# Optimization experiments

Measured on AMD Instinct MI355X. Metric: run time of the kernel, lower is better.

Reference implementation:

```python
import jax, jax.numpy as jnp
import numpy as np

B, D, R = 256, 4096, 16
MAX_R = 2 * R - 1  # static upper bound on radius; per-row steps masked by r_mask


def setup_inputs() -> dict:
    key = jax.random.key(0)
    kx, kw, kb = jax.random.split(key, 3)
    x = (jax.random.uniform(kx, (B, D)) < 0.5).astype(jnp.float32)  # random bits
    A = jax.random.normal(kw, (D, D), dtype=jnp.float32) * 0.01
    W = (A + A.T) * 0.5  # symmetric quadratic coupling
    bias = jax.random.normal(kb, (D,), dtype=jnp.float32) * 0.1
    return {"x": x, "W": W, "bias": bias}


def reference(x, W, bias):
    # energy model: score(x) = 0.5 * x' W x + b' x  (per batch row)
    score_fn = lambda z: 0.5 * jnp.einsum('bd,de,be->b', z, W, z) + z @ bias
    grad_fn = jax.grad(lambda z: score_fn(z).sum())

    key = jax.random.key(42)
    k_rad, k_samp, k_acc = jax.random.split(key, 3)
    radius = jax.random.randint(k_rad, (B, 1), 1, 2 * R)
    r_mask = (jnp.arange(MAX_R)[None, :] < radius).astype(x.dtype)  # [B, MAX_R]

    score_x = score_fn(x)                                  # [B]
    grad_x = jax.lax.stop_gradient(grad_fn(x))             # detach as in torch
    score_change_x = (1.0 - 2.0 * x) * grad_x * 0.5        # [B, D] proposal logits

    b_idx = jnp.arange(B)

    def body(carry, inp):
        cur_x, blocked = carry
        k, m = inp  # per-step RNG key, per-step mask column [B]
        idx = jax.random.categorical(k, score_change_x + blocked)  # multinomial w/ zeroed probs
        cur_bits = cur_x[b_idx, idx]
        cur_x = cur_x.at[b_idx, idx].set(m * (1.0 - cur_bits) + (1.0 - m) * cur_bits)
        blocked = blocked.at[b_idx, idx].set(-jnp.inf)  # prob_x[b, idx] = 0
        return (cur_x, blocked), idx

    keys = jax.random.split(k_samp, MAX_R)
    (y, _), idx_steps = jax.lax.scan(body, (x, jnp.zeros_like(x)), (keys, r_mask.T))
    idx_all = idx_steps.T  # [B, MAX_R]

    score_y = score_fn(y)
    grad_y = jax.lax.stop_gradient(grad_fn(y))
    score_change_y = (1.0 - 2.0 * y) * grad_y * 0.5

    # masked log-softmax tensors: step j's proposal excludes indices flipped at other steps
    oh = jax.nn.one_hot(idx_all, D, dtype=x.dtype)        # [B, MAX_R, D]
    cum = jnp.cumsum(oh, axis=1)
    before = cum - oh                                      # indices sampled at steps i < j
    after = cum[:, -1:, :] - cum                           # indices sampled at steps i > j
    change_fwd = jnp.where(before > 0, -jnp.inf, score_change_x[:, None, :])
    change_bwd = jnp.where(after > 0, -jnp.inf, score_change_y[:, None, :])

    g_fwd = jnp.take_along_axis(jax.nn.log_softmax(change_fwd, axis=-1), idx_all[:, :, None], axis=2)[..., 0]
    g_bwd = jnp.take_along_axis(jax.nn.log_softmax(change_bwd, axis=-1), idx_all[:, :, None], axis=2)[..., 0]
    log_fwd = jnp.sum(g_fwd * r_mask, axis=-1) + score_x
    log_bwd = jnp.sum(g_bwd * r_mask, axis=-1) + score_y

    log_acc = log_bwd - log_fwd
    u = jax.random.uniform(k_acc, (B,))
    accepted = (jnp.exp(log_acc) >= u).astype(x.dtype)[:, None]  # [B, 1]
    y_sg = jax.lax.stop_gradient(y)
    acc_sg = jax.lax.stop_gradient(accepted)
    return y_sg * acc_sg + (1.0 - acc_sg) * x
```

## Files before the change

### kernel.cpp

```cpp
#include <hip/hip_runtime.h>
#include <math.h>

#define BB 256
#define DD 4096
#define MAXR 31
#define NCAND 4
#define CAPG 192
#define U_THRESH 0.9778f
#define GUARD 4.0f

typedef unsigned short u16;
typedef u16 u16x8 __attribute__((ext_vector_type(8)));
typedef __bf16 bf16x8 __attribute__((ext_vector_type(8)));
typedef float f32x16 __attribute__((ext_vector_type(16)));

__device__ __forceinline__ void tf2x32(unsigned k0, unsigned k1, unsigned c0, unsigned c1,
                                       unsigned &o0, unsigned &o1) {
  unsigned ks2 = k0 ^ k1 ^ 0x1BD11BDAu;
  unsigned x0 = c0 + k0;
  unsigned x1 = c1 + k1;
#define TF_ROT(v, r) (((v) << (r)) | ((v) >> (32 - (r))))
#define TF_R(r) { x0 += x1; x1 = TF_ROT(x1, r); x1 ^= x0; }
  TF_R(13) TF_R(15) TF_R(26) TF_R(6)   x0 += k1;  x1 += ks2 + 1u;
  TF_R(17) TF_R(29) TF_R(16) TF_R(24)  x0 += ks2; x1 += k0 + 2u;
  TF_R(13) TF_R(15) TF_R(26) TF_R(6)   x0 += k0;  x1 += k1 + 3u;
  TF_R(17) TF_R(29) TF_R(16) TF_R(24)  x0 += k1;  x1 += ks2 + 4u;
  TF_R(13) TF_R(15) TF_R(26) TF_R(6)   x0 += ks2; x1 += k0 + 5u;
#undef TF_R
#undef TF_ROT
  o0 = x0; o1 = x1;
}

__device__ __forceinline__ unsigned tf_xor(unsigned k0, unsigned k1, unsigned c0, unsigned c1) {
  unsigned a, b; tf2x32(k0, k1, c0, c1, a, b); return a ^ b;
}

__device__ __forceinline__ float bits_to_unit(unsigned bits) {
  return __uint_as_float(0x3f800000u | (bits >> 9)) - 1.0f;
}

__device__ __forceinline__ void keys_of(int j, unsigned &kk0, unsigned &kk1) {
  unsigned ks0, ks1;
  tf2x32(0u, 42u, 0u, 1u, ks0, ks1);
  tf2x32(ks0, ks1, 0u, (unsigned)j, kk0, kk1);
}

__device__ __forceinline__ int radius_of(int b) {
  unsigned krad0, krad1, k10, k11, k20, k21;
  tf2x32(0u, 42u, 0u, 0u, krad0, krad1);
  tf2x32(krad0, krad1, 0u, 0u, k10, k11);
  tf2x32(krad0, krad1, 0u, 1u, k20, k21);
  unsigned hi = tf_xor(k10, k11, 0u, (unsigned)b);
  unsigned lo = tf_xor(k20, k21, 0u, (unsigned)b);
  return 1 + (int)(((hi % 31u) * 4u + (lo % 31u)) % 31u);
}

__device__ __forceinline__ float uacc_of(int b) {
  unsigned ka0, ka1;
  tf2x32(0u, 42u, 0u, 2u, ka0, ka1);
  return bits_to_unit(tf_xor(ka0, ka1, 0u, (unsigned)b));
}

__device__ __forceinline__ double dlog(double x) {
  unsigned long long ub = (unsigned long long)__double_as_longlong(x);
  int e = (int)((ub >> 52) & 0x7FFull) - 1022;
  double m = __longlong_as_double((long long)((ub & 0x000FFFFFFFFFFFFFull) | 0x3FE0000000000000ull));
  if (m < 0.70710678118654752440) { m *= 2.0; e -= 1; }
  double r = (m - 1.0) / (m + 1.0);
  double z = r * r;
  double s = fma(z, fma(z, fma(z, fma(z, fma(z, fma(z, 1.0/15.0, 1.0/13.0),
                1.0/11.0), 1.0/9.0), 1.0/7.0), 1.0/5.0), 1.0/3.0);
  double t2 = 2.0 * r;
  return fma((double)e, 0.69314718055994530942, fma(t2 * z, s, t2));
}

__device__ __forceinline__ float gumbel_from_u(float f) {
  float uu = (f == 0.0f) ? 1.17549435e-38f : f;
  float t1 = (float)dlog((double)uu);
  return -(float)dlog((double)(-t1));
}

__device__ __forceinline__ float gumbel_of(unsigned kk0, unsigned kk1, unsigned n) {
  return gumbel_from_u(bits_to_unit(tf_xor(kk0, kk1, 0u, n)));
}

__device__ __forceinline__ double blockReduce1024(double v, double* lds) {
  int t = threadIdx.x;
  #pragma unroll
  for (int off = 32; off > 0; off >>= 1) v += __shfl_down(v, off);
  __syncthreads();
  if ((t & 63) == 0) lds[t >> 6] = v;
  __syncthreads();
  double s = 0.0;
  #pragma unroll
  for (int i = 0; i < 16; i++) s += lds[i];
  return s;
}

__device__ __forceinline__ void split3(float w, u16 &h, u16 &l, u16 &q) {
  __bf16 hb = (__bf16)w;
  float r = w - (float)hb;
  __bf16 lb = (__bf16)r;
  float r2 = r - (float)lb;
  __bf16 qb = (__bf16)r2;
  h = __builtin_bit_cast(u16, hb);
  l = __builtin_bit_cast(u16, lb);
  q = __builtin_bit_cast(u16, qb);
}

__global__ __launch_bounds__(256, 2) void k_mega(
    const float* __restrict__ x, const float* __restrict__ W,
    float* __restrict__ Cpart, int klen, int ngemm,
    u16* __restrict__ flt_list, int* __restrict__ flt_cnt) {
  int t = threadIdx.x;

  if ((int)blockIdx.x < ngemm) {
    int g = blockIdx.x;
    int nt = g & 63, mt = (g >> 6) & 1, kc = g >> 7;
    int k0 = kc * klen;

    __shared__ alignas(16) u16 As[4][128][8];
    __shared__ alignas(16) u16 Bs[3][4][64][8];

    const float* xrow = x + (size_t)(mt * 128) * DD + k0;
    const float* wrow = W + (size_t)(nt * 64) * DD + k0;

    int am = t >> 2, akg = t & 3;
    int bn = t >> 2, bkg = t & 3;

    float4 aR0, aR1, aR2, aR3;
    float4 bR0, bR1;
    int nsteps = klen / 32;

    {
      const float* ap = xrow + (size_t)am * DD + akg * 8;
      aR0 = *(const float4*)ap;       aR1 = *(const float4*)(ap + 4);
      const float* ap2 = ap + (size_t)64 * DD;
      aR2 = *(const float4*)ap2;      aR3 = *(const float4*)(ap2 + 4);
      const float* wp = wrow + (size_t)bn * DD + bkg * 8;
      bR0 = *(const float4*)wp;       bR1 = *(const float4*)(wp + 4);
    }

    int wid = t >> 6, lane = t & 63;
    int wr = (wid >> 1) * 64, wc = (wid & 1) * 32;
    int lm = lane & 31, lh = lane >> 5;

    f32x16 acc[2];
    #pragma unroll
    for (int i = 0; i < 2; i++)
      #pragma unroll
      for (int r = 0; r < 16; r++) acc[i][r] = 0.0f;

    for (int s = 0; s < nsteps; s++) {
      __syncthreads();
      {
        float af32[8];
        *(float4*)&af32[0] = aR0; *(float4*)&af32[4] = aR1;
        u16x8 av;
        #pragma unroll
        for (int i = 0; i < 8; i++) av[i] = __builtin_bit_cast(u16, (__bf16)af32[i]);
        *(u16x8*)&As[akg][am][0] = av;
        *(float4*)&af32[0] = aR2; *(float4*)&af32[4] = aR3;
        #pragma unroll
        for (int i = 0; i < 8; i++) av[i] = __builtin_bit_cast(u16, (__bf16)af32[i]);
        *(u16x8*)&As[akg][am + 64][0] = av;
      }
      {
        float wv[8];
        *(float4*)&wv[0] = bR0; *(float4*)&wv[4] = bR1;
        u16x8 ph, pl, pq;
        #pragma unroll
        for (int i = 0; i < 8; i++) {
          u16 hh, ll, qq;
          split3(wv[i], hh, ll, qq);
          ph[i] = hh; pl[i] = ll; pq[i] = qq;
        }
        *(u16x8*)&Bs[0][bkg][bn][0] = ph;
        *(u16x8*)&Bs[1][bkg][bn][0] = pl;
        *(u16x8*)&Bs[2][bkg][bn][0] = pq;
      }
      __syncthreads();
      if (s + 1 < nsteps) {
        int kk = (s + 1) * 32;
        const float* ap = xrow + (size_t)am * DD + kk + akg * 8;
        aR0 = *(const float4*)ap;       aR1 = *(const float4*)(ap + 4);
        const float* ap2 = ap + (size_t)64 * DD;
        aR2 = *(const float4*)ap2;      aR3 = *(const float4*)(ap2 + 4);
        const float* wp = wrow + (size_t)bn * DD + kk + bkg * 8;
        bR0 = *(const float4*)wp;       bR1 = *(const float4*)(wp + 4);
      }
      bf16x8 af[2][2];
      #pragma unroll
      for (int mf = 0; mf < 2; mf++)
        #pragma unroll
        for (int h = 0; h < 2; h++)
          af[mf][h] = *(const bf16x8*)&As[2 * h + lh][wr + mf * 32 + lm][0];
      __builtin_amdgcn_s_setprio(1);
      #pragma unroll
      for (int p = 0; p < 3; p++) {
        bf16x8 b0 = *(const bf16x8*)&Bs[p][lh][wc + lm][0];
        bf16x8 b1 = *(const bf16x8*)&Bs[p][2 + lh][wc + lm][0];
        #pragma unroll
        for (int mf = 0; mf < 2; mf++) {
          acc[mf] = __builtin_amdgcn_mfma_f32_32x32x16_bf16(af[mf][0], b0, acc[mf], 0, 0, 0);
          acc[mf] = __builtin_amdgcn_mfma_f32_32x32x16_bf16(af[mf][1], b1, acc[mf], 0, 0, 0);
        }
      }
      __builtin_amdgcn_s_setprio(0);
    }

    float* Cp = Cpart + (size_t)kc * ((size_t)BB * DD);
    #pragma unroll
    for (int mf = 0; mf < 2; mf++) {
      int col   = nt * 64 + wc + lm;
      int rbase = mt * 128 + wr + mf * 32 + 4 * lh;
      #pragma unroll
      for (int r = 0; r < 16; r++) {
        int row = rbase + (r & 3) + 8 * (r >> 2);
        Cp[(size_t)row * DD + col] = acc[mf][r];
      }
    }
  } else {
    int fb = (int)blockIdx.x - ngemm;
    int b = fb / MAXR, j = fb % MAXR;
    unsigned kk0, kk1;
    keys_of(j, kk0, kk1);
    unsigned base_c = (unsigned)(b * DD);
    const unsigned KMIN = (unsigned)ceil((double)U_THRESH * 8388608.0);

    __shared__ int fcnt;
    __shared__ u16 fl[CAPG];
    if (t == 0) fcnt = 0;
    __syncthreads();

    #pragma unroll
    for (int p = 0; p < 16; p++) {
      int d = t + 256 * p;
      unsigned bits = tf_xor(kk0, kk1, 0u, base_c + (unsigned)d);
      if ((bits >> 9) >= KMIN) {
        int pos = atomicAdd(&fcnt, 1);
        if (pos < CAPG) fl[pos] = (u16)d;
      }
    }
    __syncthreads();
    int n = fcnt;
    if (t == 0) flt_cnt[fb] = n;
    int nstore = n < CAPG ? n : CAPG;
    if (t < nstore) flt_list[(size_t)fb * CAPG + t] = fl[t];
  }
}

__global__ __launch_bounds__(1024) void k_tail(
    const float* __restrict__ Cpart, const float* __restrict__ bias,
    const float* __restrict__ x, const float* __restrict__ W,
    const u16* __restrict__ flt_list, const int* __restrict__ flt_cnt,
    float* __restrict__ out, int KS) {
  int b = blockIdx.x, t = threadIdx.x;

  __shared__ float sc_lds[DD];
  __shared__ float gr_lds[DD];
  __shared__ double redbuf[16];
  __shared__ float lmx[16];
  __shared__ float ls_v[16];
  __shared__ int   ls_i[16];
  __shared__ float win_v[4];
  __shared__ int   win_i[4];
  __shared__ int   cand_lds[MAXR][NCAND];
  __shared__ int   fb_list[MAXR];
  __shared__ int   nfb_s;
  __shared__ int   fidx[MAXR];
  __shared__ float fsgn[MAXR];
  __shared__ unsigned mask[DD / 32];
  __shared__ int   pick_s;
  __shared__ int   nf_s;
  __shared__ float scmax_s;
  __shared__ double score_x_s, score_y_s, Ssum_s, Tsum_s;
  __shared__ float scx_s[MAXR], scy_s[MAXR];
  __shared__ float accf;

  int d0 = t * 4;
  size_t o = (size_t)b * DD + d0;
  float a0 = 0.f, a1 = 0.f, a2 = 0.f, a3 = 0.f;
  for (int kc = 0; kc < KS; kc++) {
    float4 c = *(const float4*)&Cpart[(size_t)kc * BB * DD + o];
    a0 += c.x; a1 += c.y; a2 += c.z; a3 += c.w;
  }
  float4 bv4 = *(const float4*)&bias[d0];
  float4 xv4 = *(const float4*)&x[o];
  float gg[4] = { a0 + bv4.x, a1 + bv4.y, a2 + bv4.z, a3 + bv4.w };
  float xx[4] = { xv4.x, xv4.y, xv4.z, xv4.w };
  float bb[4] = { bv4.x, bv4.y, bv4.z, bv4.w };
  float scv[4];
  double s1 = 0.0, s2 = 0.0;
  float mx = -INFINITY;
  #pragma unroll
  for (int k = 0; k < 4; k++) {
    scv[k] = (1.0f - 2.0f * xx[k]) * gg[k] * 0.5f;
    mx = fmaxf(mx, scv[k]);
    s1 += (double)xx[k] * (double)gg[k];
    s2 += (double)xx[k] * (double)bb[k];
  }
  *(float4*)&sc_lds[d0] = *(float4*)&scv[0];
  *(float4*)&gr_lds[d0] = *(float4*)&gg[0];
  if (t < 128) mask[t] = 0u;
  if (t == 0) { nf_s = radius_of(b); nfb_s = 0; }
  double sx = exp((double)scv[0]) + exp((double)scv[1]) + exp((double)scv[2]) + exp((double)scv[3]);
  double S1 = blockReduce1024(s1, redbuf);
  double S2 = blockReduce1024(s2, redbuf);
  double Sv = blockReduce1024(sx, redbuf);
  #pragma unroll
  for (int off = 32; off > 0; off >>= 1) mx = fmaxf(mx, __shfl_down(mx, off));
  __syncthreads();
  if ((t & 63) == 0) lmx[t >> 6] = mx;
  __syncthreads();
  if (t == 0) {
    float m = lmx[0];
    #pragma unroll
    for (int i = 1; i < 16; i++) m = fmaxf(m, lmx[i]);
    score_x_s = 0.5 * (S1 + S2);
    scmax_s = m;
    Ssum_s = Sv;
  }
  __syncthreads();

  int g = t >> 8, tg = t & 255;
  float scmax_l = scmax_s;
  for (int jj = 0; jj < 8; jj++) {
    int j = jj * 4 + g;
    bool active = (j < MAXR);
    unsigned kk0 = 0, kk1 = 0;
    int n = 0;
    if (active) {
      keys_of(j, kk0, kk1);
      n = flt_cnt[b * MAXR + j];
    }
    bool fastok = active && !(n > CAPG || n < NCAND);
    float v = -INFINITY; int di = 0x7FFFFFFF;
    bool dead = true;
    if (fastok && tg < n) {
      int d = (int)flt_list[(size_t)(b * MAXR + j) * CAPG + tg];
      float f = bits_to_unit(tf_xor(kk0, kk1, 0u, (unsigned)(b * DD) + (unsigned)d));
      v = sc_lds[d] + gumbel_from_u(f);
      di = d;
      dead = false;
    }
    float v4 = -INFINITY;
    for (int r = 0; r < NCAND; r++) {
      float bv = dead ? -INFINITY : v;
      int   bi = dead ? 0x7FFFFFFF : di;
      #pragma unroll
      for (int off = 32; off > 0; off >>= 1) {
        float ov = __shfl_down(bv, off);
        int   oi = __shfl_down(bi, off);
        if (ov > bv || (ov == bv && oi < bi)) { bv = ov; bi = oi; }
      }
      if ((t & 63) == 0) { ls_v[t >> 6] = bv; ls_i[t >> 6] = bi; }
      __syncthreads();
      if (tg == 0 && fastok) {
        float fv = ls_v[4 * g]; int fi = ls_i[4 * g];
        #pragma unroll
        for (int w = 1; w < 4; w++)
          if (ls_v[4 * g + w] > fv || (ls_v[4 * g + w] == fv && ls_i[4 * g + w] < fi)) { fv = ls_v[4 * g + w]; fi = ls_i[4 * g + w]; }
        win_v[g] = fv; win_i[g] = fi;
        cand_lds[j][r] = fi;
      }
      __syncthreads();
      if (fastok) {
        v4 = win_v[g];
        if (di == win_i[g]) dead = true;
      }
    }
    if (active && tg == 0) {
      bool needfb = !fastok || (v4 < scmax_l + GUARD);
      if (needfb) fb_list[atomicAdd(&nfb_s, 1)] = j;
    }
    __syncthreads();
  }

  int nfb = nfb_s;
  for (int fi = 0; fi < nfb; fi++) {
    int j = fb_list[fi];
    unsigned kk0, kk1;
    keys_of(j, kk0, kk1);
    float vq[4]; int dq[4];
    unsigned alive = 0xFu;
    #pragma unroll
    for (int q = 0; q < 4; q++) {
      int d = t * 4 + q;
      vq[q] = sc_lds[d] + gumbel_of(kk0, kk1, (unsigned)(b * DD + d));
      dq[q] = d;
    }
    for (int r = 0; r < NCAND; r++) {
      float lv = -INFINITY; int li = 0x7FFFFFFF;
      #pragma unroll
      for (int q = 0; q < 4; q++)
        if (((alive >> q) & 1u) && (vq[q] > lv || (vq[q] == lv && dq[q] < li))) { lv = vq[q]; li = dq[q]; }
      #pragma unroll
      for (int off = 32; off > 0; off >>= 1) {
        float ov = __shfl_down(lv, off);
        int   oi = __shfl_down(li, off);
        if (ov > lv || (ov == lv && oi < li)) { lv = ov; li = oi; }
      }
      if ((t & 63) == 0) { ls_v[t >> 6] = lv; ls_i[t >> 6] = li; }
      __syncthreads();
      if (t == 0) {
        float fv = ls_v[0]; int fi2 = ls_i[0];
        #pragma unroll
        for (int w = 1; w < 16; w++)
          if (ls_v[w] > fv || (ls_v[w] == fv && ls_i[w] < fi2)) { fv = ls_v[w]; fi2 = ls_i[w]; }
        cand_lds[j][r] = fi2;
        win_i[0] = fi2;
      }
      __syncthreads();
      int wi = win_i[0];
      #pragma unroll
      for (int q = 0; q < 4; q++) if (dq[q] == wi) alive &= ~(1u << q);
    }
    __syncthreads();
  }

  int jdone = 0;
  while (true) {
    if (t == 0) {
      int j = jdone;
      while (j < MAXR) {
        int pick = -1;
        #pragma unroll
        for (int r = 0; r < NCAND; r++) {
          int idx = cand_lds[j][r];
          if (pick < 0 && !((mask[idx >> 5] >> (idx & 31)) & 1u)) pick = idx;
        }
        if (pick < 0) break;
        fidx[j] = pick;
        mask[pick >> 5] |= (1u << (pick & 31));
        j++;
      }
      pick_s = j;
    }
    __syncthreads();
    int jf = pick_s;
    if (jf >= MAXR) break;
    {
      unsigned kk0, kk1;
      keys_of(jf, kk0, kk1);
      float lv = -INFINITY; int li = 0x7FFFFFFF;
      #pragma unroll
      for (int q = 0; q < 4; q++) {
        int d = t * 4 + q;
        if ((mask[d >> 5] >> (d & 31)) & 1u) continue;
        float vv = sc_lds[d] + gumbel_of(kk0, kk1, (unsigned)(b * DD + d));
        if (vv > lv || (vv == lv && d < li)) { lv = vv; li = d; }
      }
      #pragma unroll
      for (int off = 32; off > 0; off >>= 1) {
        float ov = __shfl_down(lv, off);
        int   oi = __shfl_down(li, off);
        if (ov > lv || (ov == lv && oi < li)) { lv = ov; li = oi; }
      }
      if ((t & 63) == 0) { ls_v[t >> 6] = lv; ls_i[t >> 6] = li; }
      __syncthreads();
      if (t == 0) {
        float fv = ls_v[0]; int fi2 = ls_i[0];
        #pragma unroll
        for (int w = 1; w < 16; w++)
          if (ls_v[w] > fv || (ls_v[w] == fv && ls_i[w] < fi2)) { fv = ls_v[w]; fi2 = ls_i[w]; }
        fidx[jf] = fi2;
        mask[fi2 >> 5] |= (1u << (fi2 & 31));
      }
      __syncthreads();
    }
    jdone = jf + 1;
  }

  int nf = nf_s;
  if (t < nf) fsgn[t] = 1.0f - 2.0f * x[(size_t)b * DD + fidx[t]];
  __syncthreads();

  float gd[4] = { gr_lds[d0], gr_lds[d0 + 1], gr_lds[d0 + 2], gr_lds[d0 + 3] };
  float yy[4] = { xx[0], xx[1], xx[2], xx[3] };
  for (int jj = 0; jj < nf; jj++) {
    int fd = fidx[jj];
    float s = fsgn[jj];
    float4 wv = *(const float4*)&W[(size_t)fd * DD + d0];
    gd[0] = fmaf(s, wv.x, gd[0]);
    gd[1] = fmaf(s, wv.y, gd[1]);
    gd[2] = fmaf(s, wv.z, gd[2]);
    gd[3] = fmaf(s, wv.w, gd[3]);
    int r = fd - d0;
    if (r >= 0 && r < 4) yy[r] = 1.0f - xx[r];
  }
  float scy[4];
  double t1 = 0.0, t2 = 0.0;
  #pragma unroll
  for (int k = 0; k < 4; k++) {
    scy[k] = (1.0f - 2.0f * yy[k]) * gd[k] * 0.5f;
    t1 += (double)yy[k] * (double)gd[k];
    t2 += (double)yy[k] * (double)bb[k];
  }
  double sy = exp((double)scy[0]) + exp((double)scy[1]) + exp((double)scy[2]) + exp((double)scy[3]);
  __syncthreads();
  *(float4*)&gr_lds[d0] = *(float4*)&scy[0];
  double T1 = blockReduce1024(t1, redbuf);
  double T2 = blockReduce1024(t2, redbuf);
  double Tv = blockReduce1024(sy, redbuf);
  if (t == 0) { score_y_s = 0.5 * (T1 + T2); Tsum_s = Tv; }
  __syncthreads();

  if (t < MAXR) {
    int id = fidx[t];
    scx_s[t] = sc_lds[id];
    scy_s[t] = gr_lds[id];
  }
  __syncthreads();
  if (t < 32) {
    int lane = t;
    double S = Ssum_s, T = Tsum_s;
    double ex = (t < MAXR) ? exp((double)scx_s[t]) : 0.0;
    double scn = ex;
    #pragma unroll
    for (int off = 1; off < 32; off <<= 1) {
      double ov = __shfl_up(scn, off);
      if (lane >= off) scn += ov;
    }
    double pre = scn - ex;
    double gf = (t < nf) ? ((double)scx_s[t] - dlog(S - pre)) : 0.0;
    double ey = (t < MAXR) ? exp((double)scy_s[t]) : 0.0;
    double scn2 = ey;
    #pragma unroll
    for (int off = 1; off < 32; off <<= 1) {
      double ov = __shfl_down(scn2, off);
      if (lane + off < 32) scn2 += ov;
    }
    double suf = scn2 - ey;
    double gb = (t < nf) ? ((double)scy_s[t] - dlog(T - suf)) : 0.0;
    #pragma unroll
    for (int off = 16; off > 0; off >>= 1) {
      gf += __shfl_down(gf, off);
      gb += __shfl_down(gb, off);
    }
    if (t == 0) {
      double log_acc = (gb + score_y_s) - (gf + score_x_s);
      accf = (exp(log_acc) >= (double)uacc_of(b)) ? 1.0f : 0.0f;
    }
  }
  __syncthreads();
  float a = accf;
  float4 ov4;
  ov4.x = a * yy[0] + (1.0f - a) * xx[0];
  ov4.y = a * yy[1] + (1.0f - a) * xx[1];
  ov4.z = a * yy[2] + (1.0f - a) * xx[2];
  ov4.w = a * yy[3] + (1.0f - a) * xx[3];
  *(float4*)&out[o] = ov4;
}

extern "C" void kernel_launch(void* const* d_in, const int* in_sizes, int n_in,
                              void* d_out, int out_size, void* d_ws, size_t ws_size,
                              hipStream_t stream) {
  const float* x    = (const float*)d_in[0];
  const float* W    = (const float*)d_in[1];
  const float* bias = (const float*)d_in[2];
  float* out = (float*)d_out;
  char* ws = (char*)d_ws;
  const size_t MB = 1ull << 20;

  u16*    flt_list = (u16*)(ws + 0*MB);
  int*    flt_cnt  = (int*)(ws + 3*MB);
  float*  Cpart    = (float*)(ws + 4*MB);

  size_t base = 4*MB;
  int KS = 1;
  if      (ws_size >= base + 16*MB) KS = 4;
  else if (ws_size >= base +  8*MB) KS = 2;

  int NG = 64 * 2 * KS;

  k_mega<<<NG + BB*MAXR, 256, 0, stream>>>(x, W, Cpart, DD/KS, NG, flt_list, flt_cnt);
  k_tail<<<BB, 1024, 0, stream>>>(Cpart, bias, x, W, flt_list, flt_cnt, out, KS);
}
```

Measured before the change: 239.5 us.

## Split mega kernel into filter and GEMM launches; wave-per-step candidate selection

The combined GEMM+filter kernel is split into two separate launches, k_filter then k_gemm, and the setprio hints around the MFMA loop are dropped. In k_tail, top-NCAND candidate selection now gives each wave its own proposal step, using xor-shuffle reductions over three values per lane. This replaces the four-wave groups that needed block-wide syncs on every round. It removes many __syncthreads from the tail but adds a kernel launch and loses the overlap of filter blocks with GEMM blocks.

```diff
diff --git a/kernel.cpp b/kernel.cpp
--- a/kernel.cpp
+++ b/kernel.cpp
@@ -108,146 +108,144 @@
   q = __builtin_bit_cast(u16, qb);
 }
 
-__global__ __launch_bounds__(256, 2) void k_mega(
+__global__ __launch_bounds__(256, 2) void k_gemm(
     const float* __restrict__ x, const float* __restrict__ W,
-    float* __restrict__ Cpart, int klen, int ngemm,
-    u16* __restrict__ flt_list, int* __restrict__ flt_cnt) {
+    float* __restrict__ Cpart, int klen) {
   int t = threadIdx.x;
-
-  if ((int)blockIdx.x < ngemm) {
-    int g = blockIdx.x;
-    int nt = g & 63, mt = (g >> 6) & 1, kc = g >> 7;
-    int k0 = kc * klen;
-
-    __shared__ alignas(16) u16 As[4][128][8];
-    __shared__ alignas(16) u16 Bs[3][4][64][8];
-
-    const float* xrow = x + (size_t)(mt * 128) * DD + k0;
-    const float* wrow = W + (size_t)(nt * 64) * DD + k0;
-
-    int am = t >> 2, akg = t & 3;
-    int bn = t >> 2, bkg = t & 3;
-
-    float4 aR0, aR1, aR2, aR3;
-    float4 bR0, bR1;
-    int nsteps = klen / 32;
-
+  int g = blockIdx.x;
+  int nt = g & 63, mt = (g >> 6) & 1, kc = g >> 7;
+  int k0 = kc * klen;
+
+  __shared__ alignas(16) u16 As[4][128][8];
+  __shared__ alignas(16) u16 Bs[3][4][64][8];
+
+  const float* xrow = x + (size_t)(mt * 128) * DD + k0;
+  const float* wrow = W + (size_t)(nt * 64) * DD + k0;
+
+  int am = t >> 2, akg = t & 3;
+  int bn = t >> 2, bkg = t & 3;
+
+  float4 aR0, aR1, aR2, aR3;
+  float4 bR0, bR1;
+  int nsteps = klen / 32;
+
+  {
+    const float* ap = xrow + (size_t)am * DD + akg * 8;
+    aR0 = *(const float4*)ap;       aR1 = *(const float4*)(ap + 4);
+    const float* ap2 = ap + (size_t)64 * DD;
+    aR2 = *(const float4*)ap2;      aR3 = *(const float4*)(ap2 + 4);
+    const float* wp = wrow + (size_t)bn * DD + bkg * 8;
+    bR0 = *(const float4*)wp;       bR1 = *(const float4*)(wp + 4);
+  }
+
+  int wid = t >> 6, lane = t & 63;
+  int wr = (wid >> 1) * 64, wc = (wid & 1) * 32;
+  int lm = lane & 31, lh = lane >> 5;
+
+  f32x16 acc[2];
+  #pragma unroll
+  for (int i = 0; i < 2; i++)
+    #pragma unroll
+    for (int r = 0; r < 16; r++) acc[i][r] = 0.0f;
+
+  for (int s = 0; s < nsteps; s++) {
+    __syncthreads();
     {
-      const float* ap = xrow + (size_t)am * DD + akg * 8;
+      float af32[8];
+      *(float4*)&af32[0] = aR0; *(float4*)&af32[4] = aR1;
+      u16x8 av;
+      #pragma unroll
+      for (int i = 0; i < 8; i++) av[i] = __builtin_bit_cast(u16, (__bf16)af32[i]);
+      *(u16x8*)&As[akg][am][0] = av;
+      *(float4*)&af32[0] = aR2; *(float4*)&af32[4] = aR3;
+      #pragma unroll
+      for (int i = 0; i < 8; i++) av[i] = __builtin_bit_cast(u16, (__bf16)af32[i]);
+      *(u16x8*)&As[akg][am + 64][0] = av;
+    }
+    {
+      float wv[8];
+      *(float4*)&wv[0] = bR0; *(float4*)&wv[4] = bR1;
+      u16x8 ph, pl, pq;
+      #pragma unroll
+      for (int i = 0; i < 8; i++) {
+        u16 hh, ll, qq;
+        split3(wv[i], hh, ll, qq);
+        ph[i] = hh; pl[i] = ll; pq[i] = qq;
+      }
+      *(u16x8*)&Bs[0][bkg][bn][0] = ph;
+      *(u16x8*)&Bs[1][bkg][bn][0] = pl;
+      *(u16x8*)&Bs[2][bkg][bn][0] = pq;
+    }
+    __syncthreads();
+    if (s + 1 < nsteps) {
+      int kk = (s + 1) * 32;
+      const float* ap = xrow + (size_t)am * DD + kk + akg * 8;
       aR0 = *(const float4*)ap;       aR1 = *(const float4*)(ap + 4);
       const float* ap2 = ap + (size_t)64 * DD;
       aR2 = *(const float4*)ap2;      aR3 = *(const float4*)(ap2 + 4);
-      const float* wp = wrow + (size_t)bn * DD + bkg * 8;
+      const float* wp = wrow + (size_t)bn * DD + kk + bkg * 8;
       bR0 = *(const float4*)wp;       bR1 = *(const float4*)(wp + 4);
     }
-
-    int wid = t >> 6, lane = t & 63;
-    int wr = (wid >> 1) * 64, wc = (wid & 1) * 32;
-    int lm = lane & 31, lh = lane >> 5;
-
-    f32x16 acc[2];
-    #pragma unroll
-    for (int i = 0; i < 2; i++)
-      #pragma unroll
-      for (int r = 0; r < 16; r++) acc[i][r] = 0.0f;
-
-    for (int s = 0; s < nsteps; s++) {
-      __syncthreads();
-      {
-        float af32[8];
-        *(float4*)&af32[0] = aR0; *(float4*)&af32[4] = aR1;
-        u16x8 av;
-        #pragma unroll
-        for (int i = 0; i < 8; i++) av[i] = __builtin_bit_cast(u16, (__bf16)af32[i]);
-        *(u16x8*)&As[akg][am][0] = av;
-        *(float4*)&af32[0] = aR2; *(float4*)&af32[4] = aR3;
-        #pragma unroll
-        for (int i = 0; i < 8; i++) av[i] = __builtin_bit_cast(u16, (__bf16)af32[i]);
-        *(u16x8*)&As[akg][am + 64][0] = av;
-      }
-      {
-        float wv[8];
-        *(float4*)&wv[0] = bR0; *(float4*)&wv[4] = bR1;
-        u16x8 ph, pl, pq;
-        #pragma unroll
-        for (int i = 0; i < 8; i++) {
-          u16 hh, ll, qq;
-          split3(wv[i], hh, ll, qq);
-          ph[i] = hh; pl[i] = ll; pq[i] = qq;
-        }
-        *(u16x8*)&Bs[0][bkg][bn][0] = ph;
-        *(u16x8*)&Bs[1][bkg][bn][0] = pl;
-        *(u16x8*)&Bs[2][bkg][bn][0] = pq;
-      }
-      __syncthreads();
-      if (s + 1 < nsteps) {
-        int kk = (s + 1) * 32;
-        const float* ap = xrow + (size_t)am * DD + kk + akg * 8;
-        aR0 = *(const float4*)ap;       aR1 = *(const float4*)(ap + 4);
-        const float* ap2 = ap + (size_t)64 * DD;
-        aR2 = *(const float4*)ap2;      aR3 = *(const float4*)(ap2 + 4);
-        const float* wp = wrow + (size_t)bn * DD + kk + bkg * 8;
-        bR0 = *(const float4*)wp;       bR1 = *(const float4*)(wp + 4);
-      }
-      bf16x8 af[2][2];
-      #pragma unroll
-      for (int mf = 0; mf < 2; mf++)
-        #pragma unroll
-        for (int h = 0; h < 2; h++)
-          af[mf][h] = *(const bf16x8*)&As[2 * h + lh][wr + mf * 32 + lm][0];
-      __builtin_amdgcn_s_setprio(1);
-      #pragma unroll
-      for (int p = 0; p < 3; p++) {
-        bf16x8 b0 = *(const bf16x8*)&Bs[p][lh][wc + lm][0];
-        bf16x8 b1 = *(const bf16x8*)&Bs[p][2 + lh][wc + lm][0];
-        #pragma unroll
-        for (int mf = 0; mf < 2; mf++) {
-          acc[mf] = __builtin_amdgcn_mfma_f32_32x32x16_bf16(af[mf][0], b0, acc[mf], 0, 0, 0);
-          acc[mf] = __builtin_amdgcn_mfma_f32_32x32x16_bf16(af[mf][1], b1, acc[mf], 0, 0, 0);
-        }
-      }
-      __builtin_amdgcn_s_setprio(0);
-    }
-
-    float* Cp = Cpart + (size_t)kc * ((size_t)BB * DD);
-    #pragma unroll
-    for (int mf = 0; mf < 2; mf++) {
-      int col   = nt * 64 + wc + lm;
-      int rbase = mt * 128 + wr + mf * 32 + 4 * lh;
-      #pragma unroll
-      for (int r = 0; r < 16; r++) {
-        int row = rbase + (r & 3) + 8 * (r >> 2);
-        Cp[(size_t)row * DD + col] = acc[mf][r];
-      }
-    }
-  } else {
-    int fb = (int)blockIdx.x - ngemm;
-    int b = fb / MAXR, j = fb % MAXR;
-    unsigned kk0, kk1;
-    keys_of(j, kk0, kk1);
-    unsigned base_c = (unsigned)(b * DD);
-    const unsigned KMIN = (unsigned)ceil((double)U_THRESH * 8388608.0);
-
-    __shared__ int fcnt;
-    __shared__ u16 fl[CAPG];
-    if (t == 0) fcnt = 0;
-    __syncthreads();
-
-    #pragma unroll
-    for (int p = 0; p < 16; p++) {
-      int d = t + 256 * p;
-      unsigned bits = tf_xor(kk0, kk1, 0u, base_c + (unsigned)d);
-      if ((bits >> 9) >= KMIN) {
-        int pos = atomicAdd(&fcnt, 1);
-        if (pos < CAPG) fl[pos] = (u16)d;
-      }
-    }
-    __syncthreads();
-    int n = fcnt;
-    if (t == 0) flt_cnt[fb] = n;
-    int nstore = n < CAPG ? n : CAPG;
-    if (t < nstore) flt_list[(size_t)fb * CAPG + t] = fl[t];
-  }
+    bf16x8 af[2][2];
+    #pragma unroll
+    for (int mf = 0; mf < 2; mf++)
+      #pragma unroll
+      for (int h = 0; h < 2; h++)
+        af[mf][h] = *(const bf16x8*)&As[2 * h + lh][wr + mf * 32 + lm][0];
+    #pragma unroll
+    for (int p = 0; p < 3; p++) {
+      bf16x8 b0 = *(const bf16x8*)&Bs[p][lh][wc + lm][0];
+      bf16x8 b1 = *(const bf16x8*)&Bs[p][2 + lh][wc + lm][0];
+      #pragma unroll
+      for (int mf = 0; mf < 2; mf++) {
+        acc[mf] = __builtin_amdgcn_mfma_f32_32x32x16_bf16(af[mf][0], b0, acc[mf], 0, 0, 0);
+        acc[mf] = __builtin_amdgcn_mfma_f32_32x32x16_bf16(af[mf][1], b1, acc[mf], 0, 0, 0);
+      }
+    }
+  }
+
+  float* Cp = Cpart + (size_t)kc * ((size_t)BB * DD);
+  #pragma unroll
+  for (int mf = 0; mf < 2; mf++) {
+    int col   = nt * 64 + wc + lm;
+    int rbase = mt * 128 + wr + mf * 32 + 4 * lh;
+    #pragma unroll
+    for (int r = 0; r < 16; r++) {
+      int row = rbase + (r & 3) + 8 * (r >> 2);
+      Cp[(size_t)row * DD + col] = acc[mf][r];
+    }
+  }
+}
+
+__global__ __launch_bounds__(256) void k_filter(
+    u16* __restrict__ flt_list, int* __restrict__ flt_cnt) {
+  int t = threadIdx.x;
+  int fb = blockIdx.x;
+  int b = fb / MAXR, j = fb % MAXR;
+  unsigned kk0, kk1;
+  keys_of(j, kk0, kk1);
+  unsigned base_c = (unsigned)(b * DD);
+  const unsigned KMIN = (unsigned)ceil((double)U_THRESH * 8388608.0);
+
+  __shared__ int fcnt;
+  __shared__ u16 fl[CAPG];
+  if (t == 0) fcnt = 0;
+  __syncthreads();
+
+  #pragma unroll
+  for (int p = 0; p < 16; p++) {
+    int d = t + 256 * p;
+    unsigned bits = tf_xor(kk0, kk1, 0u, base_c + (unsigned)d);
+    if ((bits >> 9) >= KMIN) {
+      int pos = atomicAdd(&fcnt, 1);
+      if (pos < CAPG) fl[pos] = (u16)d;
+    }
+  }
+  __syncthreads();
+  int n = fcnt;
+  if (t == 0) flt_cnt[fb] = n;
+  int nstore = n < CAPG ? n : CAPG;
+  if (t < nstore) flt_list[(size_t)fb * CAPG + t] = fl[t];
 }
 
 __global__ __launch_bounds__(1024) void k_tail(
@@ -263,7 +261,6 @@
   __shared__ float lmx[16];
   __shared__ float ls_v[16];
   __shared__ int   ls_i[16];
-  __shared__ float win_v[4];
   __shared__ int   win_i[4];
   __shared__ int   cand_lds[MAXR][NCAND];
   __shared__ int   fb_list[MAXR];
@@ -323,59 +320,56 @@
   }
   __syncthreads();
 
-  int g = t >> 8, tg = t & 255;
-  float scmax_l = scmax_s;
-  for (int jj = 0; jj < 8; jj++) {
-    int j = jj * 4 + g;
-    bool active = (j < MAXR);
-    unsigned kk0 = 0, kk1 = 0;
-    int n = 0;
-    if (active) {
-      keys_of(j, kk0, kk1);
-      n = flt_cnt[b * MAXR + j];
-    }
-    bool fastok = active && !(n > CAPG || n < NCAND);
-    float v = -INFINITY; int di = 0x7FFFFFFF;
-    bool dead = true;
-    if (fastok && tg < n) {
-      int d = (int)flt_list[(size_t)(b * MAXR + j) * CAPG + tg];
-      float f = bits_to_unit(tf_xor(kk0, kk1, 0u, (unsigned)(b * DD) + (unsigned)d));
-      v = sc_lds[d] + gumbel_from_u(f);
-      di = d;
-      dead = false;
-    }
-    float v4 = -INFINITY;
-    for (int r = 0; r < NCAND; r++) {
-      float bv = dead ? -INFINITY : v;
-      int   bi = dead ? 0x7FFFFFFF : di;
-      #pragma unroll
-      for (int off = 32; off > 0; off >>= 1) {
-        float ov = __shfl_down(bv, off);
-        int   oi = __shfl_down(bi, off);
-        if (ov > bv || (ov == bv && oi < bi)) { bv = ov; bi = oi; }
-      }
-      if ((t & 63) == 0) { ls_v[t >> 6] = bv; ls_i[t >> 6] = bi; }
-      __syncthreads();
-      if (tg == 0 && fastok) {
-        float fv = ls_v[4 * g]; int fi = ls_i[4 * g];
-        #pragma unroll
-        for (int w = 1; w < 4; w++)
-          if (ls_v[4 * g + w] > fv || (ls_v[4 * g + w] == fv && ls_i[4 * g + w] < fi)) { fv = ls_v[4 * g + w]; fi = ls_i[4 * g + w]; }
-        win_v[g] = fv; win_i[g] = fi;
-        cand_lds[j][r] = fi;
-      }
-      __syncthreads();
-      if (fastok) {
-        v4 = win_v[g];
-        if (di == win_i[g]) dead = true;
-      }
-    }
-    if (active && tg == 0) {
-      bool needfb = !fastok || (v4 < scmax_l + GUARD);
-      if (needfb) fb_list[atomicAdd(&nfb_s, 1)] = j;
-    }
-    __syncthreads();
-  }
+  {
+    int wv = t >> 6, ln = t & 63;
+    float scmax_l = scmax_s;
+    for (int pass = 0; pass < 2; pass++) {
+      int j = pass * 16 + wv;
+      if (j < MAXR) {
+        unsigned kk0, kk1;
+        keys_of(j, kk0, kk1);
+        int n = flt_cnt[b * MAXR + j];
+        bool fastok = !(n > CAPG || n < NCAND);
+        float v4 = -INFINITY;
+        if (fastok) {
+          const u16* fl = &flt_list[(size_t)(b * MAXR + j) * CAPG];
+          float vv[3]; int dd[3]; unsigned alive = 0u;
+          #pragma unroll
+          for (int q = 0; q < 3; q++) {
+            int idx = ln + 64 * q;
+            if (idx < n) {
+              int d = (int)fl[idx];
+              float f = bits_to_unit(tf_xor(kk0, kk1, 0u, (unsigned)(b * DD) + (unsigned)d));
+              vv[q] = sc_lds[d] + gumbel_from_u(f);
+              dd[q] = d;
+              alive |= 1u << q;
+            } else { vv[q] = -INFINITY; dd[q] = 0x7FFFFFFF; }
+          }
+          for (int r = 0; r < NCAND; r++) {
+            float bv = -INFINITY; int bi = 0x7FFFFFFF;
+            #pragma unroll
+            for (int q = 0; q < 3; q++)
+              if (((alive >> q) & 1u) && (vv[q] > bv || (vv[q] == bv && dd[q] < bi))) { bv = vv[q]; bi = dd[q]; }
+            #pragma unroll
+            for (int off = 1; off < 64; off <<= 1) {
+              float ov = __shfl_xor(bv, off);
+              int   oi = __shfl_xor(bi, off);
+              if (ov > bv || (ov == bv && oi < bi)) { bv = ov; bi = oi; }
+            }
+            if (ln == 0) cand_lds[j][r] = bi;
+            v4 = bv;
+            #pragma unroll
+            for (int q = 0; q < 3; q++) if (dd[q] == bi) alive &= ~(1u << q);
+          }
+        }
+        if (ln == 0) {
+          bool needfb = !fastok || (v4 < scmax_l + GUARD);
+          if (needfb) fb_list[atomicAdd(&nfb_s, 1)] = j;
+        }
+      }
+    }
+  }
+  __syncthreads();
 
   int nfb = nfb_s;
   for (int fi = 0; fi < nfb; fi++) {
@@ -574,6 +568,7 @@
 
   int NG = 64 * 2 * KS;
 
-  k_mega<<<NG + BB*MAXR, 256, 0, stream>>>(x, W, Cpart, DD/KS, NG, flt_list, flt_cnt);
-  k_tail<<<BB, 1024, 0, stream>>>(Cpart, bias, x, W, flt_list, flt_cnt, out, KS);
-}
+  k_filter<<<BB*MAXR, 256, 0, stream>>>(flt_list, flt_cnt);
+  k_gemm  <<<NG, 256, 0, stream>>>(x, W, Cpart, DD/KS);
+  k_tail  <<<BB, 1024, 0, stream>>>(Cpart, bias, x, W, flt_list, flt_cnt, out, KS);
+}
```

New measurement: 238.2 us. No clear change (-0.5%).
